# Kernel tuning notes

Measured on AMD Instinct MI355X. Metric: run time of the kernel, lower is better.

Reference implementation:

```python
import jax, jax.numpy as jnp
import numpy as np

B, STATE_DIM, HIDDEN, ACTION_DIM = 262144, 128, 256, 8


def setup_inputs() -> dict:
    key = jax.random.key(0)
    ks = jax.random.split(key, 5)
    state = jax.random.normal(ks[0], (B, STATE_DIM), dtype=jnp.float32)
    # torch init: weight.data.normal_(0, 0.01); biases left at default -> zeros here
    W1 = jax.random.normal(ks[1], (HIDDEN, STATE_DIM), dtype=jnp.float32) * 0.01
    b1 = jnp.zeros((HIDDEN,), dtype=jnp.float32)
    W2 = jax.random.normal(ks[2], (HIDDEN, HIDDEN), dtype=jnp.float32) * 0.01
    b2 = jnp.zeros((HIDDEN,), dtype=jnp.float32)
    W3 = jax.random.normal(ks[3], (2 * ACTION_DIM, HIDDEN), dtype=jnp.float32) * 0.01
    b3 = jnp.zeros((2 * ACTION_DIM,), dtype=jnp.float32)
    # reparameterized noise for torch.normal(u, s): sample = u + |s| * eps
    eps = jax.random.normal(ks[4], (B, ACTION_DIM), dtype=jnp.float32)
    return {"state": state, "W1": W1, "b1": b1, "W2": W2, "b2": b2,
            "W3": W3, "b3": b3, "eps": eps}


def reference(state, W1, b1, W2, b2, W3, b3, eps):
    x = state.reshape(-1, STATE_DIM)
    h = jax.nn.relu(x @ W1.T + b1)
    h = jax.nn.relu(h @ W2.T + b2)
    n = h @ W3.T + b3                       # [B, 2*ACTION_DIM]
    u = n[:, :ACTION_DIM]                   # mean
    s = jnp.abs(n[:, ACTION_DIM:])          # std (abs as in np.abs)
    action = jax.nn.sigmoid(u + s * eps)    # sigmoid(normal(u, s))
    return (action * 8 + 1).astype(jnp.int32)  # (action*8+1).int(), per row
```

## Files before the change

### kernel.cpp

```cpp
#include <hip/hip_runtime.h>
#include <math.h>

#define NB  262144
#define SD  128
#define HID 256
#define AD  8
#define RT  16

#define W1T_OFF 0
#define W2T_OFF (SD*HID)
#define W3T_OFF (W2T_OFF + HID*HID)
#define B1_OFF  (W3T_OFF + HID*2*AD)
#define B2_OFF  (B1_OFF + HID)
#define B3_OFF  (B2_OFF + HID)
#define WS_FLOATS (B3_OFF + 2*AD)

__global__ __launch_bounds__(256) void prep_weights(
    const float* __restrict__ W1, const float* __restrict__ b1,
    const float* __restrict__ W2, const float* __restrict__ b2,
    const float* __restrict__ W3, const float* __restrict__ b3,
    float* __restrict__ ws) {
  int stride = gridDim.x * blockDim.x;
  for (int i = blockIdx.x * blockDim.x + threadIdx.x; i < WS_FLOATS; i += stride) {
    float v;
    if (i < W2T_OFF) {
      int k = i >> 8, j = i & 255;
      v = W1[j * SD + k];
    } else if (i < W3T_OFF) {
      int t = i - W2T_OFF;
      int k = t >> 8, j = t & 255;
      v = W2[j * HID + k];
    } else if (i < B1_OFF) {
      int t = i - W3T_OFF;
      int k = t >> 4, j = t & 15;
      v = W3[j * HID + k];
    } else if (i < B2_OFF) {
      v = b1[i - B1_OFF];
    } else if (i < B3_OFF) {
      v = b2[i - B2_OFF];
    } else {
      v = b3[i - B3_OFF];
    }
    ws[i] = v;
  }
}

__global__ __launch_bounds__(256) void actor_fused(
    const float* __restrict__ state, const float* __restrict__ eps,
    const float* __restrict__ ws, int* __restrict__ out) {
  __shared__ float s_x[RT][SD];
  __shared__ float s_h1[RT][HID];
  __shared__ float s_h2[RT][HID];

  const float4* __restrict__ W1T4 = (const float4*)(ws + W1T_OFF);
  const float4* __restrict__ W2T4 = (const float4*)(ws + W2T_OFF);
  const float*  __restrict__ W3T  = ws + W3T_OFF;

  const int tid = threadIdx.x;
  const long rowbase = (long)blockIdx.x * RT;

  {
    const float4* st4 = (const float4*)(state + rowbase * SD);
    float4* sx4 = (float4*)&s_x[0][0];
    #pragma unroll
    for (int i = 0; i < (RT * SD / 4) / 256; ++i) {
      int idx = tid + i * 256;
      sx4[idx] = st4[idx];
    }
  }
  __syncthreads();

  const int rg = tid >> 6;
  const int cg = tid & 63;
  const int r0 = rg * 4;

  {
    float acc[4][4];
    #pragma unroll
    for (int r = 0; r < 4; ++r)
      #pragma unroll
      for (int c = 0; c < 4; ++c) acc[r][c] = 0.0f;

    for (int k = 0; k < SD; ++k) {
      float x[4];
      #pragma unroll
      for (int r = 0; r < 4; ++r) x[r] = s_x[r0 + r][k];
      float4 w = W1T4[k * 64 + cg];
      #pragma unroll
      for (int r = 0; r < 4; ++r) {
        acc[r][0] = fmaf(x[r], w.x, acc[r][0]);
        acc[r][1] = fmaf(x[r], w.y, acc[r][1]);
        acc[r][2] = fmaf(x[r], w.z, acc[r][2]);
        acc[r][3] = fmaf(x[r], w.w, acc[r][3]);
      }
    }
    float4 bb = ((const float4*)(ws + B1_OFF))[cg];
    #pragma unroll
    for (int r = 0; r < 4; ++r) {
      float4 v;
      v.x = acc[r][0] + bb.x; v.y = acc[r][1] + bb.y;
      v.z = acc[r][2] + bb.z; v.w = acc[r][3] + bb.w;
      v.x = v.x > 0.0f ? v.x : 0.0f;
      v.y = v.y > 0.0f ? v.y : 0.0f;
      v.z = v.z > 0.0f ? v.z : 0.0f;
      v.w = v.w > 0.0f ? v.w : 0.0f;
      ((float4*)&s_h1[r0 + r][0])[cg] = v;
    }
  }
  __syncthreads();

  {
    float acc[4][4];
    #pragma unroll
    for (int r = 0; r < 4; ++r)
      #pragma unroll
      for (int c = 0; c < 4; ++c) acc[r][c] = 0.0f;

    for (int k = 0; k < HID; ++k) {
      float x[4];
      #pragma unroll
      for (int r = 0; r < 4; ++r) x[r] = s_h1[r0 + r][k];
      float4 w = W2T4[k * 64 + cg];
      #pragma unroll
      for (int r = 0; r < 4; ++r) {
        acc[r][0] = fmaf(x[r], w.x, acc[r][0]);
        acc[r][1] = fmaf(x[r], w.y, acc[r][1]);
        acc[r][2] = fmaf(x[r], w.z, acc[r][2]);
        acc[r][3] = fmaf(x[r], w.w, acc[r][3]);
      }
    }
    float4 bb = ((const float4*)(ws + B2_OFF))[cg];
    #pragma unroll
    for (int r = 0; r < 4; ++r) {
      float4 v;
      v.x = acc[r][0] + bb.x; v.y = acc[r][1] + bb.y;
      v.z = acc[r][2] + bb.z; v.w = acc[r][3] + bb.w;
      v.x = v.x > 0.0f ? v.x : 0.0f;
      v.y = v.y > 0.0f ? v.y : 0.0f;
      v.z = v.z > 0.0f ? v.z : 0.0f;
      v.w = v.w > 0.0f ? v.w : 0.0f;
      ((float4*)&s_h2[r0 + r][0])[cg] = v;
    }
  }
  __syncthreads();

  {
    const int r3 = tid >> 4;
    const int c3 = tid & 15;
    float acc = 0.0f;
    for (int k = 0; k < HID; ++k)
      acc = fmaf(s_h2[r3][k], W3T[k * (2 * AD) + c3], acc);
    float n = acc + ws[B3_OFF + c3];

    float partner = __shfl_xor(n, 8, 64);
    if (c3 < AD) {
      long grow = rowbase + r3;
      float sa = fabsf(partner);
      float ev = eps[grow * AD + c3];
      float t  = __fmul_rn(sa, ev);
      float z  = __fadd_rn(n, t);
      float e  = (float)exp(-(double)z);
      float d  = __fadd_rn(1.0f, e);
      float act = 1.0f / d;
      float q  = act * 8.0f;
      float w  = __fadd_rn(q, 1.0f);
      out[grow * AD + c3] = (int)w;
    }
  }
}

extern "C" void kernel_launch(void* const* d_in, const int* in_sizes, int n_in,
                              void* d_out, int out_size, void* d_ws, size_t ws_size,
                              hipStream_t stream) {
  const float* state = (const float*)d_in[0];
  const float* W1    = (const float*)d_in[1];
  const float* b1    = (const float*)d_in[2];
  const float* W2    = (const float*)d_in[3];
  const float* b2    = (const float*)d_in[4];
  const float* W3    = (const float*)d_in[5];
  const float* b3    = (const float*)d_in[6];
  const float* eps   = (const float*)d_in[7];
  int*   out = (int*)d_out;
  float* ws  = (float*)d_ws;

  hipLaunchKernelGGL(prep_weights, dim3(128), dim3(256), 0, stream,
                     W1, b1, W2, b2, W3, b3, ws);
  hipLaunchKernelGGL(actor_fused, dim3(NB / RT), dim3(256), 0, stream,
                     state, eps, ws, out);
}
```

Measured before the change: 1.056 ms.

## Give each wavefront 8 rows, broadcast activations via readlane and packed FMA

Each wavefront now handles 8 rows on its own. Layer-1 and layer-2 activations stay in registers and are broadcast across lanes with readlane as scalar operands to v_pk_fma_f32, which removes the shared-memory staging of x and h1 and the block-wide barriers. Only h2 goes through padded shared memory for the final layer. W3 and b3 are repacked so that each lane computes the mean and std pair for one action, which removes the cross-lane shuffle. The block tile grows to 32 rows with a launch-bounds occupancy hint. In exchange, register pressure rises and readlane/SGPR traffic could serialize the inner loops.

```diff
diff --git a/kernel.cpp b/kernel.cpp
--- a/kernel.cpp
+++ b/kernel.cpp
@@ -5,15 +5,16 @@
 #define SD  128
 #define HID 256
 #define AD  8
-#define RT  16
+
+typedef float v2f __attribute__((ext_vector_type(2)));
 
 #define W1T_OFF 0
 #define W2T_OFF (SD*HID)
-#define W3T_OFF (W2T_OFF + HID*HID)
-#define B1_OFF  (W3T_OFF + HID*2*AD)
+#define W3P_OFF (W2T_OFF + HID*HID)
+#define B1_OFF  (W3P_OFF + HID*2*AD)
 #define B2_OFF  (B1_OFF + HID)
-#define B3_OFF  (B2_OFF + HID)
-#define WS_FLOATS (B3_OFF + 2*AD)
+#define B3P_OFF (B2_OFF + HID)
+#define WS_FLOATS (B3P_OFF + 2*AD)
 
 __global__ __launch_bounds__(256) void prep_weights(
     const float* __restrict__ W1, const float* __restrict__ b1,
@@ -26,146 +27,163 @@
     if (i < W2T_OFF) {
       int k = i >> 8, j = i & 255;
       v = W1[j * SD + k];
-    } else if (i < W3T_OFF) {
+    } else if (i < W3P_OFF) {
       int t = i - W2T_OFF;
       int k = t >> 8, j = t & 255;
       v = W2[j * HID + k];
     } else if (i < B1_OFF) {
-      int t = i - W3T_OFF;
-      int k = t >> 4, j = t & 15;
-      v = W3[j * HID + k];
+      int t = i - W3P_OFF;
+      int k = t >> 4, a = (t >> 1) & 7, h = t & 1;
+      v = W3[(a + 8 * h) * HID + k];
     } else if (i < B2_OFF) {
       v = b1[i - B1_OFF];
-    } else if (i < B3_OFF) {
+    } else if (i < B3P_OFF) {
       v = b2[i - B2_OFF];
     } else {
-      v = b3[i - B3_OFF];
+      int t = i - B3P_OFF;
+      v = b3[(t >> 1) + 8 * (t & 1)];
     }
     ws[i] = v;
   }
 }
 
-__global__ __launch_bounds__(256) void actor_fused(
+__device__ __forceinline__ float rdl(float v, int lane) {
+  return __int_as_float(__builtin_amdgcn_readlane(__float_as_int(v), lane));
+}
+
+__device__ __forceinline__ v2f pkfma(v2f a_sgpr, v2f b, v2f c) {
+  asm("v_pk_fma_f32 %0, %1, %2, %0" : "+v"(c) : "s"(a_sgpr), "v"(b));
+  return c;
+}
+
+__global__ __launch_bounds__(256, 4) void actor_fused(
     const float* __restrict__ state, const float* __restrict__ eps,
     const float* __restrict__ ws, int* __restrict__ out) {
-  __shared__ float s_x[RT][SD];
-  __shared__ float s_h1[RT][HID];
-  __shared__ float s_h2[RT][HID];
+  __shared__ float s_h2[32][264];
+
+  const int tid  = threadIdx.x;
+  const int lane = tid & 63;
+  const int wv   = tid >> 6;
+  const long wrow = (long)blockIdx.x * 32 + wv * 8;
 
   const float4* __restrict__ W1T4 = (const float4*)(ws + W1T_OFF);
   const float4* __restrict__ W2T4 = (const float4*)(ws + W2T_OFF);
-  const float*  __restrict__ W3T  = ws + W3T_OFF;
-
-  const int tid = threadIdx.x;
-  const long rowbase = (long)blockIdx.x * RT;
-
+  const v2f*    __restrict__ W3P  = (const v2f*)(ws + W3P_OFF);
+
+  v2f xr[8];
+  #pragma unroll
+  for (int r = 0; r < 8; ++r)
+    xr[r] = *(const v2f*)(state + (wrow + r) * SD + 2 * lane);
+
+  v2f acc[8][2];
+  #pragma unroll
+  for (int r = 0; r < 8; ++r) { acc[r][0] = (v2f)0.0f; acc[r][1] = (v2f)0.0f; }
+
+  #pragma unroll 2
+  for (int k0 = 0; k0 < SD; k0 += 4) {
+    float4 w[4];
+    #pragma unroll
+    for (int j = 0; j < 4; ++j) w[j] = W1T4[(k0 + j) * 64 + lane];
+    #pragma unroll
+    for (int j = 0; j < 4; ++j) {
+      const int src = (k0 >> 1) + (j >> 1);
+      v2f wlo = {w[j].x, w[j].y};
+      v2f whi = {w[j].z, w[j].w};
+      #pragma unroll
+      for (int r = 0; r < 8; ++r) {
+        float x = rdl((j & 1) ? xr[r].y : xr[r].x, src);
+        v2f xs = {x, x};
+        acc[r][0] = pkfma(xs, wlo, acc[r][0]);
+        acc[r][1] = pkfma(xs, whi, acc[r][1]);
+      }
+    }
+  }
+
+  float h1[8][4];
   {
-    const float4* st4 = (const float4*)(state + rowbase * SD);
-    float4* sx4 = (float4*)&s_x[0][0];
-    #pragma unroll
-    for (int i = 0; i < (RT * SD / 4) / 256; ++i) {
-      int idx = tid + i * 256;
-      sx4[idx] = st4[idx];
-    }
-  }
-  __syncthreads();
-
-  const int rg = tid >> 6;
-  const int cg = tid & 63;
-  const int r0 = rg * 4;
+    float4 bb = ((const float4*)(ws + B1_OFF))[lane];
+    #pragma unroll
+    for (int r = 0; r < 8; ++r) {
+      float v0 = acc[r][0].x + bb.x, v1 = acc[r][0].y + bb.y;
+      float v2 = acc[r][1].x + bb.z, v3 = acc[r][1].y + bb.w;
+      h1[r][0] = v0 > 0.0f ? v0 : 0.0f;
+      h1[r][1] = v1 > 0.0f ? v1 : 0.0f;
+      h1[r][2] = v2 > 0.0f ? v2 : 0.0f;
+      h1[r][3] = v3 > 0.0f ? v3 : 0.0f;
+    }
+  }
+
+  #pragma unroll
+  for (int r = 0; r < 8; ++r) { acc[r][0] = (v2f)0.0f; acc[r][1] = (v2f)0.0f; }
+
+  #pragma unroll 2
+  for (int k0 = 0; k0 < HID; k0 += 4) {
+    float4 w[4];
+    #pragma unroll
+    for (int j = 0; j < 4; ++j) w[j] = W2T4[(k0 + j) * 64 + lane];
+    const int src = k0 >> 2;
+    #pragma unroll
+    for (int j = 0; j < 4; ++j) {
+      v2f wlo = {w[j].x, w[j].y};
+      v2f whi = {w[j].z, w[j].w};
+      #pragma unroll
+      for (int r = 0; r < 8; ++r) {
+        float x = rdl(h1[r][j], src);
+        v2f xs = {x, x};
+        acc[r][0] = pkfma(xs, wlo, acc[r][0]);
+        acc[r][1] = pkfma(xs, whi, acc[r][1]);
+      }
+    }
+  }
 
   {
-    float acc[4][4];
-    #pragma unroll
-    for (int r = 0; r < 4; ++r)
-      #pragma unroll
-      for (int c = 0; c < 4; ++c) acc[r][c] = 0.0f;
-
-    for (int k = 0; k < SD; ++k) {
-      float x[4];
-      #pragma unroll
-      for (int r = 0; r < 4; ++r) x[r] = s_x[r0 + r][k];
-      float4 w = W1T4[k * 64 + cg];
-      #pragma unroll
-      for (int r = 0; r < 4; ++r) {
-        acc[r][0] = fmaf(x[r], w.x, acc[r][0]);
-        acc[r][1] = fmaf(x[r], w.y, acc[r][1]);
-        acc[r][2] = fmaf(x[r], w.z, acc[r][2]);
-        acc[r][3] = fmaf(x[r], w.w, acc[r][3]);
-      }
-    }
-    float4 bb = ((const float4*)(ws + B1_OFF))[cg];
-    #pragma unroll
-    for (int r = 0; r < 4; ++r) {
-      float4 v;
-      v.x = acc[r][0] + bb.x; v.y = acc[r][1] + bb.y;
-      v.z = acc[r][2] + bb.z; v.w = acc[r][3] + bb.w;
-      v.x = v.x > 0.0f ? v.x : 0.0f;
-      v.y = v.y > 0.0f ? v.y : 0.0f;
-      v.z = v.z > 0.0f ? v.z : 0.0f;
-      v.w = v.w > 0.0f ? v.w : 0.0f;
-      ((float4*)&s_h1[r0 + r][0])[cg] = v;
-    }
-  }
-  __syncthreads();
+    float4 bb = ((const float4*)(ws + B2_OFF))[lane];
+    #pragma unroll
+    for (int r = 0; r < 8; ++r) {
+      float4 hv;
+      hv.x = acc[r][0].x + bb.x; hv.y = acc[r][0].y + bb.y;
+      hv.z = acc[r][1].x + bb.z; hv.w = acc[r][1].y + bb.w;
+      hv.x = hv.x > 0.0f ? hv.x : 0.0f;
+      hv.y = hv.y > 0.0f ? hv.y : 0.0f;
+      hv.z = hv.z > 0.0f ? hv.z : 0.0f;
+      hv.w = hv.w > 0.0f ? hv.w : 0.0f;
+      *(float4*)&s_h2[wv * 8 + r][4 * lane] = hv;
+    }
+  }
 
   {
-    float acc[4][4];
-    #pragma unroll
-    for (int r = 0; r < 4; ++r)
-      #pragma unroll
-      for (int c = 0; c < 4; ++c) acc[r][c] = 0.0f;
-
-    for (int k = 0; k < HID; ++k) {
-      float x[4];
-      #pragma unroll
-      for (int r = 0; r < 4; ++r) x[r] = s_h1[r0 + r][k];
-      float4 w = W2T4[k * 64 + cg];
-      #pragma unroll
-      for (int r = 0; r < 4; ++r) {
-        acc[r][0] = fmaf(x[r], w.x, acc[r][0]);
-        acc[r][1] = fmaf(x[r], w.y, acc[r][1]);
-        acc[r][2] = fmaf(x[r], w.z, acc[r][2]);
-        acc[r][3] = fmaf(x[r], w.w, acc[r][3]);
-      }
-    }
-    float4 bb = ((const float4*)(ws + B2_OFF))[cg];
-    #pragma unroll
-    for (int r = 0; r < 4; ++r) {
-      float4 v;
-      v.x = acc[r][0] + bb.x; v.y = acc[r][1] + bb.y;
-      v.z = acc[r][2] + bb.z; v.w = acc[r][3] + bb.w;
-      v.x = v.x > 0.0f ? v.x : 0.0f;
-      v.y = v.y > 0.0f ? v.y : 0.0f;
-      v.z = v.z > 0.0f ? v.z : 0.0f;
-      v.w = v.w > 0.0f ? v.w : 0.0f;
-      ((float4*)&s_h2[r0 + r][0])[cg] = v;
-    }
-  }
-  __syncthreads();
-
-  {
-    const int r3 = tid >> 4;
-    const int c3 = tid & 15;
-    float acc = 0.0f;
-    for (int k = 0; k < HID; ++k)
-      acc = fmaf(s_h2[r3][k], W3T[k * (2 * AD) + c3], acc);
-    float n = acc + ws[B3_OFF + c3];
-
-    float partner = __shfl_xor(n, 8, 64);
-    if (c3 < AD) {
-      long grow = rowbase + r3;
-      float sa = fabsf(partner);
-      float ev = eps[grow * AD + c3];
-      float t  = __fmul_rn(sa, ev);
-      float z  = __fadd_rn(n, t);
-      float e  = (float)exp(-(double)z);
-      float d  = __fadd_rn(1.0f, e);
-      float act = 1.0f / d;
-      float q  = act * 8.0f;
-      float w  = __fadd_rn(q, 1.0f);
-      out[grow * AD + c3] = (int)w;
-    }
+    const int r3 = lane >> 3;
+    const int a  = lane & 7;
+    const float* __restrict__ h2row = &s_h2[wv * 8 + r3][0];
+    float accu = 0.0f, accs = 0.0f;
+    #pragma unroll 2
+    for (int k0 = 0; k0 < HID; k0 += 4) {
+      v2f ha = *(const v2f*)(h2row + k0);
+      v2f hb = *(const v2f*)(h2row + k0 + 2);
+      v2f wp0 = W3P[(k0 + 0) * 8 + a];
+      v2f wp1 = W3P[(k0 + 1) * 8 + a];
+      v2f wp2 = W3P[(k0 + 2) * 8 + a];
+      v2f wp3 = W3P[(k0 + 3) * 8 + a];
+      accu = fmaf(ha.x, wp0.x, accu); accs = fmaf(ha.x, wp0.y, accs);
+      accu = fmaf(ha.y, wp1.x, accu); accs = fmaf(ha.y, wp1.y, accs);
+      accu = fmaf(hb.x, wp2.x, accu); accs = fmaf(hb.x, wp2.y, accs);
+      accu = fmaf(hb.y, wp3.x, accu); accs = fmaf(hb.y, wp3.y, accs);
+    }
+    v2f b3p = ((const v2f*)(ws + B3P_OFF))[a];
+    float nu = accu + b3p.x;
+    float ns = accs + b3p.y;
+
+    long grow = wrow + r3;
+    float sa = fabsf(ns);
+    float ev = eps[grow * AD + a];
+    float t  = __fmul_rn(sa, ev);
+    float z  = __fadd_rn(nu, t);
+    float e  = (float)exp(-(double)z);
+    float d  = __fadd_rn(1.0f, e);
+    float act = 1.0f / d;
+    float q  = act * 8.0f;
+    float wq = __fadd_rn(q, 1.0f);
+    out[grow * AD + a] = (int)wq;
   }
 }
 
@@ -185,6 +203,6 @@
 
   hipLaunchKernelGGL(prep_weights, dim3(128), dim3(256), 0, stream,
                      W1, b1, W2, b2, W3, b3, ws);
-  hipLaunchKernelGGL(actor_fused, dim3(NB / RT), dim3(256), 0, stream,
+  hipLaunchKernelGGL(actor_fused, dim3(NB / 32), dim3(256), 0, stream,
                      state, eps, ws, out);
 }
```

Result: faster. 994.7 us (-5.8%).
